# Kernel tuning notes

Measured on AMD Instinct MI355X. Metric: run time of the kernel, lower is better.

## Reference

```python
import jax, jax.numpy as jnp
import numpy as np

B, T, E, D = 8, 4096, 64, 8  # batch, seq, embed_dim, head_dim (embed_dim//heads)


def setup_inputs() -> dict:
    key = jax.random.key(0)
    ks = jax.random.split(key, 7)
    scale = 1.0 / np.sqrt(E).astype(np.float32)
    return {
        "x": jax.random.normal(ks[0], (B, T, E), dtype=jnp.float32),
        "Wq": jax.random.normal(ks[1], (E, D), dtype=jnp.float32) * scale,
        "bq": jax.random.normal(ks[2], (D,), dtype=jnp.float32) * 0.01,
        "Wk": jax.random.normal(ks[3], (E, D), dtype=jnp.float32) * scale,
        "bk": jax.random.normal(ks[4], (D,), dtype=jnp.float32) * 0.01,
        "Wv": jax.random.normal(ks[5], (E, D), dtype=jnp.float32) * scale,
        "bv": jax.random.normal(ks[6], (D,), dtype=jnp.float32) * 0.01,
    }


def reference(x, Wq, bq, Wk, bk, Wv, bv):
    # q, k, v: [B, T, D]
    q = x @ Wq + bq
    k = x @ Wk + bk
    v = x @ Wv + bv
    b, t, d = k.shape
    # FAITHFUL to source: key(x).view(B, C, T) is a RESHAPE, not a transpose.
    w = q @ k.reshape(b, d, t)  # [B, T, T]
    # tril then masked_fill(w == 0, -inf): zero entries (incl. masked-out
    # upper triangle) become -inf before softmax.
    w = jnp.tril(w)
    w = jnp.where(w == 0, -jnp.inf, w)
    w = jax.nn.softmax(w / np.float32(np.sqrt(d)), axis=-1)
    return w @ v  # [B, T, D]
```

## Files before the change

### kernel.cpp

```cpp
#include <hip/hip_runtime.h>
#include <math.h>

#define BB 8
#define TT 4096
#define EE 64
#define DD 8
#define QSCALE 0.51012604f
#define CSHIFT -12.0f

typedef _Float16 half8  __attribute__((ext_vector_type(8)));
typedef _Float16 half4v __attribute__((ext_vector_type(4)));
typedef float    floatx4 __attribute__((ext_vector_type(4)));

#define VP_BATCH 65536

__global__ __launch_bounds__(256) void proj_kernel(
    const float* __restrict__ x,
    const float* __restrict__ Wq, const float* __restrict__ bq,
    const float* __restrict__ Wk, const float* __restrict__ bk,
    const float* __restrict__ Wv, const float* __restrict__ bv,
    _Float16* __restrict__ qh, _Float16* __restrict__ ks, _Float16* __restrict__ vP)
{
    __shared__ float    xs[32][EE + 1];
    __shared__ _Float16 qsm[256];
    __shared__ _Float16 ksm[256];
    __shared__ _Float16 vsm[256];

    const int tid   = threadIdx.x;
    const int blk   = blockIdx.x;
    const int b     = blk >> 7;
    const int tbase = (blk & 127) << 2;

#pragma unroll
    for (int m2 = 0; m2 < 2; ++m2) {
        int r = (tid >> 4) + (m2 << 4);
        int c = (tid & 15) << 2;
        int t = ((r >> 2) << 9) + tbase + (r & 3);
        float4 a = *(const float4*)(x + (size_t)(b * TT + t) * EE + c);
        xs[r][c+0] = a.x; xs[r][c+1] = a.y; xs[r][c+2] = a.z; xs[r][c+3] = a.w;
    }
    __syncthreads();

    const int r = tid >> 3;
    const int d = tid & 7;
    float accq = bq[d], acck = bk[d], accv = bv[d];
#pragma unroll
    for (int e = 0; e < EE; ++e) {
        float xv = xs[r][e];
        accq = fmaf(xv, Wq[e*DD + d], accq);
        acck = fmaf(xv, Wk[e*DD + d], acck);
        accv = fmaf(xv, Wv[e*DD + d], accv);
    }
    qsm[tid] = (_Float16)(accq * QSCALE);
    ksm[((r & 3) << 6) + (d << 3) + (r >> 2)] = (_Float16)acck;
    vsm[(d << 5) + r] = (_Float16)accv;
    __syncthreads();

    const int ilow = tbase >> 6;
    const int pv_  = (tbase >> 5) & 1;
    const int g2_  = (tbase >> 2) & 3;
    const int joff = (tbase & 16) ? 4 : 0;

    if (tid < 32) {
        half8 qv = *(half8*)(qsm + tid * 8);
        *(half8*)(qh + (size_t)b*(TT*DD) + (size_t)(tid >> 2)*(512*DD)
                     + (size_t)tbase*DD + ((tid & 3) << 3)) = qv;
        half8 kv = *(half8*)(ksm + tid * 8);
        *(half8*)(ks + (size_t)b*(TT*DD) + (size_t)tbase*64 + tid * 8) = kv;
    } else if (tid >= 64 && tid < 128) {
        int idx = tid - 64, d2 = idx >> 3, g2x = idx & 7;
        half4v vv = *(half4v*)(vsm + (d2 << 5) + (g2x << 2));
        const int i_ = (g2x << 3) + ilow;
        *(half4v*)(vP + (size_t)b*VP_BATCH + (size_t)i_*1024 + pv_*512
                      + (g2_ << 7) + (d2 << 3) + joff) = vv;
    } else if (tid >= 128 && tid < 136) {
        int g2x = tid & 7;
        const int i_ = (g2x << 3) + ilow;
        half4v ones = {(_Float16)1.0f, (_Float16)1.0f, (_Float16)1.0f, (_Float16)1.0f};
        *(half4v*)(vP + (size_t)b*VP_BATCH + (size_t)i_*1024 + pv_*512
                      + (g2_ << 7) + (8 << 3) + joff) = ones;
    }
}

__global__ __launch_bounds__(512, 4) void attn_kernel(
    const _Float16* __restrict__ qh, const _Float16* __restrict__ ks,
    const _Float16* __restrict__ vP, float* __restrict__ out)
{
    __shared__ floatx4 obuf[2][8][64];

    const int lane = threadIdx.x & 63;
    const int wave = threadIdx.x >> 6;
    const int g = lane >> 4;
    const int n = lane & 15;

    const int blk = blockIdx.x;
    const int bb  = blk & 7;
    const int p   = blk >> 3;
    const int ntA = (p >> 2) + 1;
    const int ntB = ((255 - p) >> 2) + 1;
    const int r0A = p << 4;
    const int r0B = (255 - p) << 4;

    const _Float16* ksb = ks + (size_t)bb * (TT*DD);
    const _Float16* vPb = vP + (size_t)bb * VP_BATCH + (lane << 3);

    half8 qfA, qfB;
    {
        half8 z;
#pragma unroll
        for (int j = 0; j < 8; ++j) z[j] = (_Float16)0.0f;
        qfA = z; qfB = z;
        if (g == 0) {
            qfA = *(const half8*)(qh + ((size_t)bb*TT + r0A + n) * DD);
            qfB = *(const half8*)(qh + ((size_t)bb*TT + r0B + n) * DD);
        }
    }

    floatx4 oA = {0.f, 0.f, 0.f, 0.f};
    floatx4 oB = {0.f, 0.f, 0.f, 0.f};
    const floatx4 C12 = {CSHIFT, CSHIFT, CSHIFT, CSHIFT};

#define ATTN_LOOP(NT, R0, QF, OACC)                                             \
    for (int i = wave; i < (NT); i += 8) {                                      \
        const int t2base = i << 6;                                              \
        const _Float16* kp = ksb + (size_t)(t2base + n) * DD;                   \
        half8 ck0 = *(const half8*)(kp);                                        \
        half8 ck1 = *(const half8*)(kp + 16 * DD);                              \
        half8 ck2 = *(const half8*)(kp + 32 * DD);                              \
        half8 ck3 = *(const half8*)(kp + 48 * DD);                              \
        half8 va0 = *(const half8*)(vPb + (size_t)i * 1024);                    \
        half8 va1 = *(const half8*)(vPb + (size_t)i * 1024 + 512);              \
        floatx4 S[4];                                                           \
        S[0] = __builtin_amdgcn_mfma_f32_16x16x32_f16(ck0, QF, C12, 0, 0, 0);   \
        S[1] = __builtin_amdgcn_mfma_f32_16x16x32_f16(ck1, QF, C12, 0, 0, 0);   \
        S[2] = __builtin_amdgcn_mfma_f32_16x16x32_f16(ck2, QF, C12, 0, 0, 0);   \
        S[3] = __builtin_amdgcn_mfma_f32_16x16x32_f16(ck3, QF, C12, 0, 0, 0);   \
        if (t2base + 63 > (R0)) {                                               \
            const int lim = (R0) + n - t2base - (g << 2);                       \
            _Pragma("unroll")                                                   \
            for (int s = 0; s < 4; ++s)                                         \
                _Pragma("unroll")                                               \
                for (int rr = 0; rr < 4; ++rr)                                  \
                    if ((s << 4) + rr > lim) S[s][rr] = -INFINITY;              \
        }                                                                       \
        int lo[4], hi[4];                                                       \
        _Pragma("unroll")                                                       \
        for (int s = 0; s < 4; ++s) {                                           \
            float p0 = __builtin_amdgcn_exp2f(S[s][0]);                         \
            float p1 = __builtin_amdgcn_exp2f(S[s][1]);                         \
            float p2 = __builtin_amdgcn_exp2f(S[s][2]);                         \
            float p3 = __builtin_amdgcn_exp2f(S[s][3]);                         \
            lo[s] = __builtin_bit_cast(int, __builtin_amdgcn_cvt_pkrtz(p0, p1));\
            hi[s] = __builtin_bit_cast(int, __builtin_amdgcn_cvt_pkrtz(p2, p3));\
        }                                                                       \
               \
        {                                                                       \
            int4 bi; bi.x = lo[0]; bi.y = hi[0]; bi.z = lo[1]; bi.w = hi[1];    \
            half8 pb = __builtin_bit_cast(half8, bi);                           \
            OACC = __builtin_amdgcn_mfma_f32_16x16x32_f16(va0, pb, OACC, 0, 0, 0);\
        }                                                                       \
                                             \
        {                                                                       \
            int4 bi; bi.x = lo[2]; bi.y = hi[2]; bi.z = lo[3]; bi.w = hi[3];    \
            half8 pb = __builtin_bit_cast(half8, bi);                           \
            OACC = __builtin_amdgcn_mfma_f32_16x16x32_f16(va1, pb, OACC, 0, 0, 0);\
        }                                                                       \
    }

    ATTN_LOOP(ntA, r0A, qfA, oA)
    ATTN_LOOP(ntB, r0B, qfB, oB)
#undef ATTN_LOOP

    obuf[0][wave][lane] = oA;
    obuf[1][wave][lane] = oB;
    __syncthreads();

    if (wave < 2) {
        floatx4 osum = {0.f, 0.f, 0.f, 0.f};
#pragma unroll
        for (int w = 0; w < 8; ++w) osum += obuf[wave][w][lane];
        const float l    = __shfl(osum[0], 32 + n, 64);
        const float linv = 1.0f / l;
        const int   r0   = wave ? r0B : r0A;
        if (g < 2) {
            float4 res;
            res.x = osum[0] * linv; res.y = osum[1] * linv;
            res.z = osum[2] * linv; res.w = osum[3] * linv;
            *(float4*)(out + (((size_t)bb * TT + r0 + n) * DD) + (g << 2)) = res;
        }
    }
}

extern "C" void kernel_launch(void* const* d_in, const int* in_sizes, int n_in,
                              void* d_out, int out_size, void* d_ws, size_t ws_size,
                              hipStream_t stream) {
    const float* x  = (const float*)d_in[0];
    const float* Wq = (const float*)d_in[1];
    const float* bq = (const float*)d_in[2];
    const float* Wk = (const float*)d_in[3];
    const float* bk = (const float*)d_in[4];
    const float* Wv = (const float*)d_in[5];
    const float* bv = (const float*)d_in[6];
    float* out = (float*)d_out;

    _Float16* qhp = (_Float16*)d_ws;
    _Float16* ksp = qhp + (size_t)BB * TT * DD;
    _Float16* vPp = ksp + (size_t)BB * TT * DD;

    proj_kernel<<<BB * TT / 32, 256, 0, stream>>>(x, Wq, bq, Wk, bk, Wv, bv, qhp, ksp, vPp);
    attn_kernel<<<1024, 512, 0, stream>>>(qhp, ksp, vPp, out);
}
```

Baseline: 90.50 us.

## Process two 16-row query tiles per K/V load in attention kernel

Each block now handles two pairs of 32-row query blocks instead of 16-row ones, and each loaded K/V tile is reused by two query sub-tiles. The goal is to halve K/V global loads per unit of work and the per-block overhead, with the grid halved to 512 blocks. In exchange there is more register pressure, twice the shared-memory reduction buffer, and fewer blocks to spread over the CUs, which may hurt occupancy and load balance.

```diff
diff --git a/kernel.cpp b/kernel.cpp
--- a/kernel.cpp
+++ b/kernel.cpp
@@ -86,7 +86,7 @@
     const _Float16* __restrict__ qh, const _Float16* __restrict__ ks,
     const _Float16* __restrict__ vP, float* __restrict__ out)
 {
-    __shared__ floatx4 obuf[2][8][64];
+    __shared__ floatx4 obuf[4][8][64];
 
     const int lane = threadIdx.x & 63;
     const int wave = threadIdx.x >> 6;
@@ -96,40 +96,34 @@
     const int blk = blockIdx.x;
     const int bb  = blk & 7;
     const int p   = blk >> 3;
-    const int ntA = (p >> 2) + 1;
-    const int ntB = ((255 - p) >> 2) + 1;
-    const int r0A = p << 4;
-    const int r0B = (255 - p) << 4;
+    const int r0A = p << 5;
+    const int r0B = (127 - p) << 5;
+    const int ntA = (p >> 1) + 1;
+    const int ntB = ((255 - (p << 1)) >> 2) + 1;
 
     const _Float16* ksb = ks + (size_t)bb * (TT*DD);
     const _Float16* vPb = vP + (size_t)bb * VP_BATCH + (lane << 3);
 
-    half8 qfA, qfB;
+    half8 qfA0, qfA1, qfB0, qfB1;
     {
         half8 z;
 #pragma unroll
         for (int j = 0; j < 8; ++j) z[j] = (_Float16)0.0f;
-        qfA = z; qfB = z;
+        qfA0 = z; qfA1 = z; qfB0 = z; qfB1 = z;
         if (g == 0) {
-            qfA = *(const half8*)(qh + ((size_t)bb*TT + r0A + n) * DD);
-            qfB = *(const half8*)(qh + ((size_t)bb*TT + r0B + n) * DD);
+            qfA0 = *(const half8*)(qh + ((size_t)bb*TT + r0A + n) * DD);
+            qfA1 = *(const half8*)(qh + ((size_t)bb*TT + r0A + 16 + n) * DD);
+            qfB0 = *(const half8*)(qh + ((size_t)bb*TT + r0B + n) * DD);
+            qfB1 = *(const half8*)(qh + ((size_t)bb*TT + r0B + 16 + n) * DD);
         }
     }
 
-    floatx4 oA = {0.f, 0.f, 0.f, 0.f};
-    floatx4 oB = {0.f, 0.f, 0.f, 0.f};
+    floatx4 oA0 = {0.f,0.f,0.f,0.f}, oA1 = {0.f,0.f,0.f,0.f};
+    floatx4 oB0 = {0.f,0.f,0.f,0.f}, oB1 = {0.f,0.f,0.f,0.f};
     const floatx4 C12 = {CSHIFT, CSHIFT, CSHIFT, CSHIFT};
 
-#define ATTN_LOOP(NT, R0, QF, OACC)                                             \
-    for (int i = wave; i < (NT); i += 8) {                                      \
-        const int t2base = i << 6;                                              \
-        const _Float16* kp = ksb + (size_t)(t2base + n) * DD;                   \
-        half8 ck0 = *(const half8*)(kp);                                        \
-        half8 ck1 = *(const half8*)(kp + 16 * DD);                              \
-        half8 ck2 = *(const half8*)(kp + 32 * DD);                              \
-        half8 ck3 = *(const half8*)(kp + 48 * DD);                              \
-        half8 va0 = *(const half8*)(vPb + (size_t)i * 1024);                    \
-        half8 va1 = *(const half8*)(vPb + (size_t)i * 1024 + 512);              \
+#define TILE_BODY(QF, R0, OACC)                                                 \
+    {                                                                           \
         floatx4 S[4];                                                           \
         S[0] = __builtin_amdgcn_mfma_f32_16x16x32_f16(ck0, QF, C12, 0, 0, 0);   \
         S[1] = __builtin_amdgcn_mfma_f32_16x16x32_f16(ck1, QF, C12, 0, 0, 0);   \
@@ -153,13 +147,11 @@
             lo[s] = __builtin_bit_cast(int, __builtin_amdgcn_cvt_pkrtz(p0, p1));\
             hi[s] = __builtin_bit_cast(int, __builtin_amdgcn_cvt_pkrtz(p2, p3));\
         }                                                                       \
-               \
         {                                                                       \
             int4 bi; bi.x = lo[0]; bi.y = hi[0]; bi.z = lo[1]; bi.w = hi[1];    \
             half8 pb = __builtin_bit_cast(half8, bi);                           \
             OACC = __builtin_amdgcn_mfma_f32_16x16x32_f16(va0, pb, OACC, 0, 0, 0);\
         }                                                                       \
-                                             \
         {                                                                       \
             int4 bi; bi.x = lo[2]; bi.y = hi[2]; bi.z = lo[3]; bi.w = hi[3];    \
             half8 pb = __builtin_bit_cast(half8, bi);                           \
@@ -167,21 +159,38 @@
         }                                                                       \
     }
 
-    ATTN_LOOP(ntA, r0A, qfA, oA)
-    ATTN_LOOP(ntB, r0B, qfB, oB)
-#undef ATTN_LOOP
-
-    obuf[0][wave][lane] = oA;
-    obuf[1][wave][lane] = oB;
+#define ATTN_LOOP2(NT, R0LO, QF0, QF1, O0, O1)                                  \
+    for (int i = wave; i < (NT); i += 8) {                                      \
+        const int t2base = i << 6;                                              \
+        const _Float16* kp = ksb + (size_t)(t2base + n) * DD;                   \
+        half8 ck0 = *(const half8*)(kp);                                        \
+        half8 ck1 = *(const half8*)(kp + 16 * DD);                              \
+        half8 ck2 = *(const half8*)(kp + 32 * DD);                              \
+        half8 ck3 = *(const half8*)(kp + 48 * DD);                              \
+        half8 va0 = *(const half8*)(vPb + (size_t)i * 1024);                    \
+        half8 va1 = *(const half8*)(vPb + (size_t)i * 1024 + 512);              \
+        TILE_BODY(QF0, (R0LO), O0)                                              \
+        TILE_BODY(QF1, (R0LO) + 16, O1)                                         \
+    }
+
+    ATTN_LOOP2(ntA, r0A, qfA0, qfA1, oA0, oA1)
+    ATTN_LOOP2(ntB, r0B, qfB0, qfB1, oB0, oB1)
+#undef ATTN_LOOP2
+#undef TILE_BODY
+
+    obuf[0][wave][lane] = oA0;
+    obuf[1][wave][lane] = oA1;
+    obuf[2][wave][lane] = oB0;
+    obuf[3][wave][lane] = oB1;
     __syncthreads();
 
-    if (wave < 2) {
+    if (wave < 4) {
         floatx4 osum = {0.f, 0.f, 0.f, 0.f};
 #pragma unroll
         for (int w = 0; w < 8; ++w) osum += obuf[wave][w][lane];
         const float l    = __shfl(osum[0], 32 + n, 64);
         const float linv = 1.0f / l;
-        const int   r0   = wave ? r0B : r0A;
+        const int   r0   = ((wave & 2) ? r0B : r0A) + ((wave & 1) << 4);
         if (g < 2) {
             float4 res;
             res.x = osum[0] * linv; res.y = osum[1] * linv;
@@ -208,5 +217,5 @@
     _Float16* vPp = ksp + (size_t)BB * TT * DD;
 
     proj_kernel<<<BB * TT / 32, 256, 0, stream>>>(x, Wq, bq, Wk, bk, Wv, bv, qhp, ksp, vPp);
-    attn_kernel<<<1024, 512, 0, stream>>>(qhp, ksp, vPp, out);
+    attn_kernel<<<512, 512, 0, stream>>>(qhp, ksp, vPp, out);
 }
```

New measurement: 86.85 us. 4.0% less time.
